# Performance work log

Measured on AMD Instinct MI355X. Metric: run time of the kernel, lower is better.

The kernel has to match this reference:

```python
import jax, jax.numpy as jnp
import numpy as np

INPUT_DIM = 512
HIDDEN_DIM = 512
B, N = 8, 2048


def setup_inputs() -> dict:
    key = jax.random.key(0)
    ks = jax.random.split(key, 9)
    s_in = 1.0 / np.sqrt(INPUT_DIM)
    s_h = 1.0 / np.sqrt(HIDDEN_DIM)
    return {
        "X": jax.random.normal(ks[0], (B, N, INPUT_DIM), dtype=jnp.float32),
        "Wq": jax.random.uniform(ks[1], (INPUT_DIM, HIDDEN_DIM), minval=-s_in, maxval=s_in),
        "bq": jnp.zeros((HIDDEN_DIM,), jnp.float32),
        "Wk": jax.random.uniform(ks[2], (INPUT_DIM, HIDDEN_DIM), minval=-s_in, maxval=s_in),
        "bk": jnp.zeros((HIDDEN_DIM,), jnp.float32),
        "Wv": jax.random.uniform(ks[3], (INPUT_DIM, HIDDEN_DIM), minval=-s_in, maxval=s_in),
        "bv": jnp.zeros((HIDDEN_DIM,), jnp.float32),
        "Wo": jax.random.uniform(ks[4], (HIDDEN_DIM, INPUT_DIM), minval=-s_h, maxval=s_h),
        "bo": jnp.zeros((INPUT_DIM,), jnp.float32),
        "ln_gamma": jnp.ones((INPUT_DIM,), jnp.float32),
        "ln_beta": jnp.zeros((INPUT_DIM,), jnp.float32),
    }


def reference(X, Wq, bq, Wk, bk, Wv, bv, Wo, bo, ln_gamma, ln_beta):
    q = X @ Wq + bq                      # [B,N,H]
    k = X @ Wk + bk
    v = X @ Wv + bv
    scores = jnp.einsum('bnh,bmh->bnm', q, k) / jnp.sqrt(jnp.float32(HIDDEN_DIM))
    attn = jax.nn.softmax(scores, axis=-1)      # [B,N,N]
    ctx = jnp.einsum('bnm,bmh->bnh', attn, v)   # [B,N,H]
    out = ctx @ Wo + bo + X                      # residual
    mu = jnp.mean(out, axis=-1, keepdims=True)
    var = jnp.var(out, axis=-1, keepdims=True)
    normed = (out - mu) / jnp.sqrt(var + 1e-5)
    return normed * ln_gamma + ln_beta
```

## Files before the change

### kernel.cpp

```cpp
#include <hip/hip_runtime.h>
#include <cstdint>
#include <cstddef>


typedef __bf16 bf16x8 __attribute__((ext_vector_type(8)));
typedef float  f32x4  __attribute__((ext_vector_type(4)));

__device__ __forceinline__ uint16_t f2bf(float f) {
  union { float f; uint32_t u; } v; v.f = f;
  uint32_t r = v.u + 0x7FFFu + ((v.u >> 16) & 1u);
  return (uint16_t)(r >> 16);
}
__device__ __forceinline__ float bf2f(uint32_t u) {
  union { uint32_t u; float f; } v; v.u = u << 16; return v.f;
}

__device__ __forceinline__ void gld16(const uint16_t* g, uint16_t* l) {
  __builtin_amdgcn_global_load_lds(
      (__attribute__((address_space(1))) void*)(g),
      (__attribute__((address_space(3))) void*)(l), 16, 0, 0);
}

template <int MODE, int BM>
__global__ __launch_bounds__(256) void gemm_k(
    const uint16_t* __restrict__ A, const uint16_t* __restrict__ Bt,
    void* __restrict__ OutA, uint16_t* __restrict__ OutK,
    uint16_t* __restrict__ OutVT, int K, int lda, int ldb,
    const float* __restrict__ b0, const float* __restrict__ b1,
    const float* __restrict__ b2, const float* __restrict__ Xres, float scale) {
  constexpr int MT = BM / 32;
  __shared__ alignas(16) uint16_t As[2 * BM * 32];
  __shared__ alignas(16) uint16_t Bs[2 * 128 * 32];

  const int tid = threadIdx.x;
  const int w = tid >> 6, lane = tid & 63;
  const int wm = w >> 1, wn = w & 1;
  const int m0 = blockIdx.y * BM, n0 = blockIdx.x * 128;
  const int z = blockIdx.z;

  const uint16_t* Ab = A;
  const uint16_t* Bb = Bt;
  if (MODE == 1) { Ab += (size_t)z * 2048 * 512;  Bb += (size_t)z * 2048 * 512; }
  if (MODE == 2) { Ab += (size_t)z * 2048 * 2048; Bb += (size_t)z * 512 * 2048; }

  const int kc = (lane & 3) * 8;
  const int rowA = (BM == 128 ? w * 32 : w * 16);
  const int rsA = rowA + (lane >> 2);
  const int rsB = w * 32 + (lane >> 2);
  const uint16_t* gA = Ab + (size_t)(m0 + rsA) * lda + kc;
  const uint16_t* gB = Bb + (size_t)(n0 + rsB) * ldb + kc;
  uint16_t* lA0 = &As[rowA * 32];
  uint16_t* lB0 = &Bs[(w * 32) * 32];

  f32x4 acc[MT][4];
#pragma unroll
  for (int i = 0; i < MT; i++)
#pragma unroll
    for (int j = 0; j < 4; j++) acc[i][j] = (f32x4){0.f, 0.f, 0.f, 0.f};

  const int lr = lane & 15;
  const int q8 = (lane >> 4) * 8;

  for (int k0 = 0; k0 < K; k0 += 64) {
    gld16(gA + k0, lA0);
    if (BM == 128) gld16(gA + k0 + (size_t)16 * lda, lA0 + 16 * 32);
    gld16(gB + k0, lB0);
    gld16(gB + k0 + (size_t)16 * ldb, lB0 + 16 * 32);
    gld16(gA + k0 + 32, lA0 + BM * 32);
    if (BM == 128) gld16(gA + k0 + 32 + (size_t)16 * lda, lA0 + BM * 32 + 16 * 32);
    gld16(gB + k0 + 32, lB0 + 128 * 32);
    gld16(gB + k0 + 32 + (size_t)16 * ldb, lB0 + 128 * 32 + 16 * 32);
    __syncthreads();
#pragma unroll
    for (int h = 0; h < 2; h++) {
      bf16x8 af[MT], bfr[4];
#pragma unroll
      for (int t = 0; t < MT; t++)
        af[t] = *(const bf16x8*)
            &As[h * BM * 32 + (wm * (BM / 2) + t * 16 + lr) * 32 + q8];
#pragma unroll
      for (int t = 0; t < 4; t++)
        bfr[t] = *(const bf16x8*)
            &Bs[h * 128 * 32 + (wn * 64 + t * 16 + lr) * 32 + q8];
#pragma unroll
      for (int nt = 0; nt < 4; nt++)
#pragma unroll
        for (int mt = 0; mt < MT; mt++)
          acc[mt][nt] = __builtin_amdgcn_mfma_f32_16x16x32_bf16(
              af[mt], bfr[nt], acc[mt][nt], 0, 0, 0);
    }
    __syncthreads();
  }

#pragma unroll
  for (int mt = 0; mt < MT; mt++) {
#pragma unroll
    for (int nt = 0; nt < 4; nt++) {
#pragma unroll
      for (int i = 0; i < 4; i++) {
        const int row = m0 + wm * (BM / 2) + mt * 16 + (lane >> 4) * 4 + i;
        const int col = n0 + wn * 64 + nt * 16 + lr;
        const float v = acc[mt][nt][i];
        if (MODE == 0) {
          const int which = col >> 9, c = col & 511;
          if (which == 0) {
            ((uint16_t*)OutA)[(size_t)row * 512 + c] = f2bf(v + b0[c]);
          } else if (which == 1) {
            OutK[(size_t)row * 512 + c] = f2bf(v + b1[c]);
          } else {
            OutVT[(size_t)(row >> 11) * (512 * 2048) + (size_t)c * 2048 +
                  (row & 2047)] = f2bf(v + b2[c]);
          }
        } else if (MODE == 1) {
          ((uint16_t*)OutA)[(size_t)z * 2048 * 2048 + (size_t)row * 2048 + col] =
              f2bf(v * scale);
        } else if (MODE == 2) {
          ((uint16_t*)OutA)[((size_t)z * 2048 + row) * 512 + col] = f2bf(v);
        } else {
          const size_t idx = (size_t)row * 512 + col;
          ((float*)OutA)[idx] = v + b0[col] + Xres[idx];
        }
      }
    }
  }
}

__global__ __launch_bounds__(256) void cvt_x_k(const float* __restrict__ X,
                                               uint16_t* __restrict__ Xb) {
  const int i = blockIdx.x * 256 + threadIdx.x;
  const float4 f = ((const float4*)X)[i];
  uint32_t lo = (uint32_t)f2bf(f.x) | ((uint32_t)f2bf(f.y) << 16);
  uint32_t hi = (uint32_t)f2bf(f.z) | ((uint32_t)f2bf(f.w) << 16);
  ((uint2*)Xb)[i] = make_uint2(lo, hi);
}

__global__ __launch_bounds__(256) void cvt_w_k(
    const float* __restrict__ Wq, const float* __restrict__ Wk,
    const float* __restrict__ Wv, const float* __restrict__ Wo,
    uint16_t* __restrict__ Wt) {
  const int gid = blockIdx.x * 256 + threadIdx.x;
  const int n = gid >> 9, kk = gid & 511;
  const int which = n >> 9, c = n & 511;
  const float* W = (which == 0) ? Wq : (which == 1) ? Wk : (which == 2) ? Wv : Wo;
  Wt[gid] = f2bf(W[kk * 512 + c]);
}

__global__ __launch_bounds__(256) void softmax_k(uint16_t* __restrict__ S) {
  __shared__ float red[4];
  uint16_t* p = S + (size_t)blockIdx.x * 2048;
  const int tid = threadIdx.x, w = tid >> 6, lane = tid & 63;
  const uint4 raw = ((const uint4*)p)[tid];
  float x[8];
  x[0] = bf2f(raw.x & 0xFFFF); x[1] = bf2f(raw.x >> 16);
  x[2] = bf2f(raw.y & 0xFFFF); x[3] = bf2f(raw.y >> 16);
  x[4] = bf2f(raw.z & 0xFFFF); x[5] = bf2f(raw.z >> 16);
  x[6] = bf2f(raw.w & 0xFFFF); x[7] = bf2f(raw.w >> 16);
  float mx = x[0];
#pragma unroll
  for (int j = 1; j < 8; j++) mx = fmaxf(mx, x[j]);
#pragma unroll
  for (int off = 32; off >= 1; off >>= 1) mx = fmaxf(mx, __shfl_xor(mx, off));
  if (lane == 0) red[w] = mx;
  __syncthreads();
  mx = fmaxf(fmaxf(red[0], red[1]), fmaxf(red[2], red[3]));
  float e[8], s = 0.f;
#pragma unroll
  for (int j = 0; j < 8; j++) { e[j] = __expf(x[j] - mx); s += e[j]; }
#pragma unroll
  for (int off = 32; off >= 1; off >>= 1) s += __shfl_xor(s, off);
  __syncthreads();
  if (lane == 0) red[w] = s;
  __syncthreads();
  s = red[0] + red[1] + red[2] + red[3];
  const float inv = 1.f / s;
  uint32_t o0 = (uint32_t)f2bf(e[0] * inv) | ((uint32_t)f2bf(e[1] * inv) << 16);
  uint32_t o1 = (uint32_t)f2bf(e[2] * inv) | ((uint32_t)f2bf(e[3] * inv) << 16);
  uint32_t o2 = (uint32_t)f2bf(e[4] * inv) | ((uint32_t)f2bf(e[5] * inv) << 16);
  uint32_t o3 = (uint32_t)f2bf(e[6] * inv) | ((uint32_t)f2bf(e[7] * inv) << 16);
  ((uint4*)p)[tid] = make_uint4(o0, o1, o2, o3);
}

__global__ __launch_bounds__(256) void ln_k(float* __restrict__ O,
                                            const float* __restrict__ g,
                                            const float* __restrict__ b) {
  const int tid = threadIdx.x, w = tid >> 6, lane = tid & 63;
  float* p = O + ((size_t)blockIdx.x * 4 + w) * 512;
  float4 v0 = ((const float4*)p)[lane];
  float4 v1 = ((const float4*)p)[64 + lane];
  float s  = v0.x + v0.y + v0.z + v0.w + v1.x + v1.y + v1.z + v1.w;
  float sq = v0.x * v0.x + v0.y * v0.y + v0.z * v0.z + v0.w * v0.w +
             v1.x * v1.x + v1.y * v1.y + v1.z * v1.z + v1.w * v1.w;
#pragma unroll
  for (int off = 32; off >= 1; off >>= 1) {
    s += __shfl_xor(s, off);
    sq += __shfl_xor(sq, off);
  }
  const float mean = s * (1.f / 512.f);
  const float var = sq * (1.f / 512.f) - mean * mean;
  const float rstd = rsqrtf(var + 1e-5f);
  const float4 g0 = ((const float4*)g)[lane], g1 = ((const float4*)g)[64 + lane];
  const float4 b0 = ((const float4*)b)[lane], b1 = ((const float4*)b)[64 + lane];
  v0.x = (v0.x - mean) * rstd * g0.x + b0.x;
  v0.y = (v0.y - mean) * rstd * g0.y + b0.y;
  v0.z = (v0.z - mean) * rstd * g0.z + b0.z;
  v0.w = (v0.w - mean) * rstd * g0.w + b0.w;
  v1.x = (v1.x - mean) * rstd * g1.x + b1.x;
  v1.y = (v1.y - mean) * rstd * g1.y + b1.y;
  v1.z = (v1.z - mean) * rstd * g1.z + b1.z;
  v1.w = (v1.w - mean) * rstd * g1.w + b1.w;
  ((float4*)p)[lane] = v0;
  ((float4*)p)[64 + lane] = v1;
}

extern "C" void kernel_launch(void* const* d_in, const int* in_sizes, int n_in,
                              void* d_out, int out_size, void* d_ws,
                              size_t ws_size, hipStream_t stream) {
  const float* X     = (const float*)d_in[0];
  const float* Wq    = (const float*)d_in[1];
  const float* bq    = (const float*)d_in[2];
  const float* Wk    = (const float*)d_in[3];
  const float* bk    = (const float*)d_in[4];
  const float* Wv    = (const float*)d_in[5];
  const float* bv    = (const float*)d_in[6];
  const float* Wo    = (const float*)d_in[7];
  const float* bo    = (const float*)d_in[8];
  const float* gamma = (const float*)d_in[9];
  const float* beta  = (const float*)d_in[10];
  float* out = (float*)d_out;

  char* ws = (char*)d_ws;
  uint16_t* S   = (uint16_t*)(ws);
  uint16_t* Xb  = (uint16_t*)(ws);
  uint16_t* Wt  = (uint16_t*)(ws + 67108864);
  uint16_t* q   = (uint16_t*)(ws + 69206016);
  uint16_t* kb  = (uint16_t*)(ws + 85983232);
  uint16_t* vT  = (uint16_t*)(ws + 102760448);
  uint16_t* ctx = q;

  cvt_x_k<<<dim3(8192), dim3(256), 0, stream>>>(X, Xb);
  cvt_w_k<<<dim3(4096), dim3(256), 0, stream>>>(Wq, Wk, Wv, Wo, Wt);
  gemm_k<0, 128><<<dim3(12, 128, 1), dim3(256), 0, stream>>>(
      Xb, Wt, (void*)q, kb, vT, 512, 512, 512, bq, bk, bv, nullptr, 1.f);
  gemm_k<1, 128><<<dim3(16, 16, 8), dim3(256), 0, stream>>>(
      q, kb, (void*)S, nullptr, nullptr, 512, 512, 512, nullptr, nullptr,
      nullptr, nullptr, 0.044194173824159216f);
  softmax_k<<<dim3(16384), dim3(256), 0, stream>>>(S);
  gemm_k<2, 64><<<dim3(4, 32, 8), dim3(256), 0, stream>>>(
      S, vT, (void*)ctx, nullptr, nullptr, 2048, 2048, 2048, nullptr, nullptr,
      nullptr, nullptr, 1.f);
  gemm_k<3, 128><<<dim3(4, 128, 1), dim3(256), 0, stream>>>(
      ctx, Wt + 1536 * 512, (void*)out, nullptr, nullptr, 512, 512, 512, bo,
      nullptr, nullptr, X, 1.f);
  ln_k<<<dim3(4096), dim3(256), 0, stream>>>(out, gamma, beta);
}
```

Measured before the change: 338.9 us.

## Fuse softmax into QK^T epilogue and defer normalization to PV GEMM

```diff
diff --git a/kernel.cpp b/kernel.cpp
--- a/kernel.cpp
+++ b/kernel.cpp
@@ -25,8 +25,8 @@
 __global__ __launch_bounds__(256) void gemm_k(
     const uint16_t* __restrict__ A, const uint16_t* __restrict__ Bt,
     void* __restrict__ OutA, uint16_t* __restrict__ OutK,
-    uint16_t* __restrict__ OutVT, int K, int lda, int ldb,
-    const float* __restrict__ b0, const float* __restrict__ b1,
+    uint16_t* __restrict__ OutVT, float* __restrict__ rsum, int K, int lda,
+    int ldb, const float* __restrict__ b0, const float* __restrict__ b1,
     const float* __restrict__ b2, const float* __restrict__ Xres, float scale) {
   constexpr int MT = BM / 32;
   __shared__ alignas(16) uint16_t As[2 * BM * 32];
@@ -92,33 +92,72 @@
     __syncthreads();
   }
 
-#pragma unroll
-  for (int mt = 0; mt < MT; mt++) {
-#pragma unroll
-    for (int nt = 0; nt < 4; nt++) {
+  if (MODE == 1) {
+    uint16_t* Sp = (uint16_t*)OutA + (size_t)z * 2048 * 2048;
+#pragma unroll
+    for (int mt = 0; mt < MT; mt++) {
+      float rp[4] = {0.f, 0.f, 0.f, 0.f};
+#pragma unroll
+      for (int nt = 0; nt < 4; nt++) {
+#pragma unroll
+        for (int i = 0; i < 4; i++) {
+          const int row = m0 + wm * (BM / 2) + mt * 16 + (lane >> 4) * 4 + i;
+          const int col = n0 + wn * 64 + nt * 16 + lr;
+          const float e = __expf(acc[mt][nt][i] * scale);
+          Sp[(size_t)row * 2048 + col] = f2bf(e);
+          rp[i] += e;
+        }
+      }
+#pragma unroll
+      for (int i = 0; i < 4; i++) {
+        float p = rp[i];
+        p += __shfl_xor(p, 1); p += __shfl_xor(p, 2);
+        p += __shfl_xor(p, 4); p += __shfl_xor(p, 8);
+        if (lr == 0) {
+          const int row = m0 + wm * (BM / 2) + mt * 16 + (lane >> 4) * 4 + i;
+          atomicAdd(&rsum[z * 2048 + row], p);
+        }
+      }
+    }
+  } else if (MODE == 2) {
+#pragma unroll
+    for (int mt = 0; mt < MT; mt++) {
 #pragma unroll
       for (int i = 0; i < 4; i++) {
         const int row = m0 + wm * (BM / 2) + mt * 16 + (lane >> 4) * 4 + i;
-        const int col = n0 + wn * 64 + nt * 16 + lr;
-        const float v = acc[mt][nt][i];
-        if (MODE == 0) {
-          const int which = col >> 9, c = col & 511;
-          if (which == 0) {
-            ((uint16_t*)OutA)[(size_t)row * 512 + c] = f2bf(v + b0[c]);
-          } else if (which == 1) {
-            OutK[(size_t)row * 512 + c] = f2bf(v + b1[c]);
+        const float sc = 1.0f / rsum[z * 2048 + row];
+#pragma unroll
+        for (int nt = 0; nt < 4; nt++) {
+          const int col = n0 + wn * 64 + nt * 16 + lr;
+          ((uint16_t*)OutA)[((size_t)z * 2048 + row) * 512 + col] =
+              f2bf(acc[mt][nt][i] * sc);
+        }
+      }
+    }
+  } else {
+#pragma unroll
+    for (int mt = 0; mt < MT; mt++) {
+#pragma unroll
+      for (int nt = 0; nt < 4; nt++) {
+#pragma unroll
+        for (int i = 0; i < 4; i++) {
+          const int row = m0 + wm * (BM / 2) + mt * 16 + (lane >> 4) * 4 + i;
+          const int col = n0 + wn * 64 + nt * 16 + lr;
+          const float v = acc[mt][nt][i];
+          if (MODE == 0) {
+            const int which = col >> 9, c = col & 511;
+            if (which == 0) {
+              ((uint16_t*)OutA)[(size_t)row * 512 + c] = f2bf(v + b0[c]);
+            } else if (which == 1) {
+              OutK[(size_t)row * 512 + c] = f2bf(v + b1[c]);
+            } else {
+              OutVT[(size_t)(row >> 11) * (512 * 2048) + (size_t)c * 2048 +
+                    (row & 2047)] = f2bf(v + b2[c]);
+            }
           } else {
-            OutVT[(size_t)(row >> 11) * (512 * 2048) + (size_t)c * 2048 +
-                  (row & 2047)] = f2bf(v + b2[c]);
+            const size_t idx = (size_t)row * 512 + col;
+            ((float*)OutA)[idx] = v + b0[col] + Xres[idx];
           }
-        } else if (MODE == 1) {
-          ((uint16_t*)OutA)[(size_t)z * 2048 * 2048 + (size_t)row * 2048 + col] =
-              f2bf(v * scale);
-        } else if (MODE == 2) {
-          ((uint16_t*)OutA)[((size_t)z * 2048 + row) * 512 + col] = f2bf(v);
-        } else {
-          const size_t idx = (size_t)row * 512 + col;
-          ((float*)OutA)[idx] = v + b0[col] + Xres[idx];
         }
       }
     }
@@ -137,47 +176,13 @@
 __global__ __launch_bounds__(256) void cvt_w_k(
     const float* __restrict__ Wq, const float* __restrict__ Wk,
     const float* __restrict__ Wv, const float* __restrict__ Wo,
-    uint16_t* __restrict__ Wt) {
+    uint16_t* __restrict__ Wt, float* __restrict__ rsum) {
   const int gid = blockIdx.x * 256 + threadIdx.x;
+  if (gid < 16384) rsum[gid] = 0.f;
   const int n = gid >> 9, kk = gid & 511;
   const int which = n >> 9, c = n & 511;
   const float* W = (which == 0) ? Wq : (which == 1) ? Wk : (which == 2) ? Wv : Wo;
   Wt[gid] = f2bf(W[kk * 512 + c]);
-}
-
-__global__ __launch_bounds__(256) void softmax_k(uint16_t* __restrict__ S) {
-  __shared__ float red[4];
-  uint16_t* p = S + (size_t)blockIdx.x * 2048;
-  const int tid = threadIdx.x, w = tid >> 6, lane = tid & 63;
-  const uint4 raw = ((const uint4*)p)[tid];
-  float x[8];
-  x[0] = bf2f(raw.x & 0xFFFF); x[1] = bf2f(raw.x >> 16);
-  x[2] = bf2f(raw.y & 0xFFFF); x[3] = bf2f(raw.y >> 16);
-  x[4] = bf2f(raw.z & 0xFFFF); x[5] = bf2f(raw.z >> 16);
-  x[6] = bf2f(raw.w & 0xFFFF); x[7] = bf2f(raw.w >> 16);
-  float mx = x[0];
-#pragma unroll
-  for (int j = 1; j < 8; j++) mx = fmaxf(mx, x[j]);
-#pragma unroll
-  for (int off = 32; off >= 1; off >>= 1) mx = fmaxf(mx, __shfl_xor(mx, off));
-  if (lane == 0) red[w] = mx;
-  __syncthreads();
-  mx = fmaxf(fmaxf(red[0], red[1]), fmaxf(red[2], red[3]));
-  float e[8], s = 0.f;
-#pragma unroll
-  for (int j = 0; j < 8; j++) { e[j] = __expf(x[j] - mx); s += e[j]; }
-#pragma unroll
-  for (int off = 32; off >= 1; off >>= 1) s += __shfl_xor(s, off);
-  __syncthreads();
-  if (lane == 0) red[w] = s;
-  __syncthreads();
-  s = red[0] + red[1] + red[2] + red[3];
-  const float inv = 1.f / s;
-  uint32_t o0 = (uint32_t)f2bf(e[0] * inv) | ((uint32_t)f2bf(e[1] * inv) << 16);
-  uint32_t o1 = (uint32_t)f2bf(e[2] * inv) | ((uint32_t)f2bf(e[3] * inv) << 16);
-  uint32_t o2 = (uint32_t)f2bf(e[4] * inv) | ((uint32_t)f2bf(e[5] * inv) << 16);
-  uint32_t o3 = (uint32_t)f2bf(e[6] * inv) | ((uint32_t)f2bf(e[7] * inv) << 16);
-  ((uint4*)p)[tid] = make_uint4(o0, o1, o2, o3);
 }
 
 __global__ __launch_bounds__(256) void ln_k(float* __restrict__ O,
@@ -229,27 +234,28 @@
   float* out = (float*)d_out;
 
   char* ws = (char*)d_ws;
-  uint16_t* S   = (uint16_t*)(ws);
-  uint16_t* Xb  = (uint16_t*)(ws);
-  uint16_t* Wt  = (uint16_t*)(ws + 67108864);
-  uint16_t* q   = (uint16_t*)(ws + 69206016);
-  uint16_t* kb  = (uint16_t*)(ws + 85983232);
-  uint16_t* vT  = (uint16_t*)(ws + 102760448);
-  uint16_t* ctx = q;
+  uint16_t* S    = (uint16_t*)(ws);
+  uint16_t* Xb   = (uint16_t*)(ws);
+  uint16_t* Wt   = (uint16_t*)(ws + 67108864);
+  uint16_t* q    = (uint16_t*)(ws + 69206016);
+  uint16_t* kb   = (uint16_t*)(ws + 85983232);
+  uint16_t* vT   = (uint16_t*)(ws + 102760448);
+  float*    rsum = (float*)(ws + 119537664);
+  uint16_t* ctx  = q;
 
   cvt_x_k<<<dim3(8192), dim3(256), 0, stream>>>(X, Xb);
-  cvt_w_k<<<dim3(4096), dim3(256), 0, stream>>>(Wq, Wk, Wv, Wo, Wt);
+  cvt_w_k<<<dim3(4096), dim3(256), 0, stream>>>(Wq, Wk, Wv, Wo, Wt, rsum);
   gemm_k<0, 128><<<dim3(12, 128, 1), dim3(256), 0, stream>>>(
-      Xb, Wt, (void*)q, kb, vT, 512, 512, 512, bq, bk, bv, nullptr, 1.f);
+      Xb, Wt, (void*)q, kb, vT, nullptr, 512, 512, 512, bq, bk, bv, nullptr,
+      1.f);
   gemm_k<1, 128><<<dim3(16, 16, 8), dim3(256), 0, stream>>>(
-      q, kb, (void*)S, nullptr, nullptr, 512, 512, 512, nullptr, nullptr,
+      q, kb, (void*)S, nullptr, nullptr, rsum, 512, 512, 512, nullptr, nullptr,
       nullptr, nullptr, 0.044194173824159216f);
-  softmax_k<<<dim3(16384), dim3(256), 0, stream>>>(S);
   gemm_k<2, 64><<<dim3(4, 32, 8), dim3(256), 0, stream>>>(
-      S, vT, (void*)ctx, nullptr, nullptr, 2048, 2048, 2048, nullptr, nullptr,
-      nullptr, nullptr, 1.f);
+      S, vT, (void*)ctx, nullptr, nullptr, rsum, 2048, 2048, 2048, nullptr,
+      nullptr, nullptr, nullptr, 1.f);
   gemm_k<3, 128><<<dim3(4, 128, 1), dim3(256), 0, stream>>>(
-      ctx, Wt + 1536 * 512, (void*)out, nullptr, nullptr, 512, 512, 512, bo,
-      nullptr, nullptr, X, 1.f);
+      ctx, Wt + 1536 * 512, (void*)out, nullptr, nullptr, nullptr, 512, 512,
+      512, bo, nullptr, nullptr, X, 1.f);
   ln_k<<<dim3(4096), dim3(256), 0, stream>>>(out, gamma, beta);
 }
```

After: 338.0 us. Within noise of the previous version (-0.3%).
